# Kernel optimization log

Measured on AMD Instinct MI355X. Metric: run time of the kernel, lower is better.

The kernel has to match this reference:

```python
import jax, jax.numpy as jnp
import numpy as np

TEMPERATURE = 0.07
N, D, NUM_CLASSES = 8192, 1024, 128


def setup_inputs() -> dict:
    key = jax.random.key(0)
    k1, k2 = jax.random.split(key)
    embeddings = jax.random.normal(k1, (N, D), dtype=jnp.float32)
    labels = jax.random.randint(k2, (N,), 0, NUM_CLASSES, dtype=jnp.int64)
    return {"embeddings": embeddings, "labels": labels}


def reference(embeddings, labels):
    # L2-normalize rows (eps matches F.normalize default clamp of 1e-12 on the norm)
    norm = jnp.maximum(jnp.linalg.norm(embeddings, axis=-1, keepdims=True), 1e-12)
    emb = embeddings / norm
    # [N, N] similarity scaled by temperature
    sim = jnp.matmul(emb, emb.T) / TEMPERATURE
    # positive mask: same label, diagonal zeroed
    pos_mask = (labels[:, None] == labels[None, :]).astype(sim.dtype)
    pos_mask = pos_mask * (1.0 - jnp.eye(sim.shape[0], dtype=sim.dtype))
    exp_sim = jnp.exp(sim)
    sum_exp = exp_sim.sum(axis=1)              # [N]
    pos_sum = (exp_sim * pos_mask).sum(axis=1)  # [N]
    loss = -jnp.log(pos_sum / sum_exp)
    return loss.mean()
```

## Files before the change

### kernel.cpp

```cpp
#include <hip/hip_runtime.h>
#include <hip/hip_bf16.h>
#include <math.h>

#define N 8192
#define D 1024
#define BM 256
#define BK 64
#define NQUART 64
#define NFULL 512
#define NBLK (NQUART + NFULL)
#define ITERS 8

typedef __bf16 bf16_t;
typedef bf16_t bf16x4 __attribute__((ext_vector_type(4)));
typedef bf16_t bf16x8 __attribute__((ext_vector_type(8)));
typedef float f32x4 __attribute__((ext_vector_type(4)));

__global__ __launch_bounds__(256) void norm_cast(const float* __restrict__ in,
                                                 bf16_t* __restrict__ out,
                                                 float* __restrict__ sumExp,
                                                 float* __restrict__ posSum) {
    const int wave = threadIdx.x >> 6, lane = threadIdx.x & 63;
    const int row  = blockIdx.x * 4 + wave;
    const float4* src = (const float4*)(in + (size_t)row * D);
    float4 v[4];
    float ss = 0.f;
    #pragma unroll
    for (int i = 0; i < 4; ++i) {
        v[i] = src[lane + 64 * i];
        ss += v[i].x * v[i].x + v[i].y * v[i].y + v[i].z * v[i].z + v[i].w * v[i].w;
    }
    #pragma unroll
    for (int off = 32; off >= 1; off >>= 1) ss += __shfl_xor(ss, off, 64);
    const float scale = 1.0f / fmaxf(sqrtf(ss), 1e-12f);
    bf16x4* dst = (bf16x4*)(out + (size_t)row * D);
    #pragma unroll
    for (int i = 0; i < 4; ++i) {
        bf16x4 o;
        o[0] = (bf16_t)(v[i].x * scale);
        o[1] = (bf16_t)(v[i].y * scale);
        o[2] = (bf16_t)(v[i].z * scale);
        o[3] = (bf16_t)(v[i].w * scale);
        dst[lane + 64 * i] = o;
    }
    if (lane == 0) { sumExp[row] = 0.f; posSum[row] = 0.f; }
}

__global__ __launch_bounds__(512, 2) void gemm_fused(const bf16_t* __restrict__ E,
                                                     const int* __restrict__ labels,
                                                     float* __restrict__ sumExp,
                                                     float* __restrict__ posSum) {
    __shared__ bf16_t As[2][2][128 * 64];
    __shared__ bf16_t Bs[2][2][128 * 64];

    const int tid  = threadIdx.x;
    const int wave = tid >> 6;
    const int lane = tid & 63;
    const int lr   = lane & 15;
    const int q    = lane >> 4;
    const float invT = 1.0f / 0.07f;

    const int su0 = ((0 + q) ^ (lane & 7)) * 16;
    const int su1 = ((4 + q) ^ (lane & 7)) * 16;

    #define PHASE_MID() do {                                                             \
        __builtin_amdgcn_s_barrier();                                                    \
        asm volatile("s_waitcnt lgkmcnt(0)");                                            \
        __builtin_amdgcn_sched_barrier(0);                                               \
        __builtin_amdgcn_s_setprio(1);                                                   \
    } while (0)
    #define PHASE_END() do {                                                             \
        __builtin_amdgcn_s_setprio(0);                                                   \
        __builtin_amdgcn_s_barrier();                                                    \
    } while (0)

    if (blockIdx.x >= NFULL) {
        const int qb = (int)blockIdx.x - NFULL;
        const int p  = qb >> 2, qd = qb & 3;
        const int rowStart = 31 * BM + (qd >> 1) * 128;
        const int colStart = p * BM + (qd & 1) * 128;
        const int wm2 = wave >> 2;
        const int wn2 = wave & 3;
        char* Aflat = (char*)&As[0][0][0];
        char* Bflat = (char*)&Bs[0][0][0];

        f32x4 acc[4][2];
        #pragma unroll
        for (int m = 0; m < 4; ++m) { acc[m][0] = {0,0,0,0}; acc[m][1] = {0,0,0,0}; }

        const int r0 = tid >> 4;
        const int lu = (tid & 15) ^ (r0 & 7);
        const char* gA = (const char*)(E + (size_t)rowStart * D) + (size_t)r0 * 2048 + lu * 16;
        const char* gB = (const char*)(E + (size_t)colStart * D) + (size_t)r0 * 2048 + lu * 16;

        #define Q128STAGE(bi, t) do {                                                    \
            const char* ga_ = gA + (t) * 256;                                            \
            const char* gb_ = gB + (t) * 256;                                            \
            char* la_ = Aflat + (bi) * 32768 + wave * 1024;                              \
            char* lb_ = Bflat + (bi) * 32768 + wave * 1024;                              \
            _Pragma("unroll")                                                            \
            for (int g_ = 0; g_ < 4; ++g_) {                                             \
                __builtin_amdgcn_global_load_lds(                                        \
                    (const __attribute__((address_space(1))) void*)(ga_ + g_ * 32 * 2048), \
                    (__attribute__((address_space(3))) void*)(la_ + g_ * 8192), 16, 0, 0); \
                __builtin_amdgcn_global_load_lds(                                        \
                    (const __attribute__((address_space(1))) void*)(gb_ + g_ * 32 * 2048), \
                    (__attribute__((address_space(3))) void*)(lb_ + g_ * 8192), 16, 0, 0); \
            }                                                                            \
        } while (0)

        Q128STAGE(0, 0);
        asm volatile("s_waitcnt vmcnt(0)" ::: "memory");
        __builtin_amdgcn_sched_barrier(0);
        __builtin_amdgcn_s_barrier();

        #pragma unroll 1
        for (int s = 0; s < 8; ++s) {
            const int buf = s & 1;
            if (s < 7) Q128STAGE(buf ^ 1, s + 1);
            const char* aB = Aflat + buf * 32768 + (wm2 * 64 + lr) * 256;
            const char* bB = Bflat + buf * 32768 + (wn2 * 32 + lr) * 256;
            #pragma unroll
            for (int kc = 0; kc < 4; ++kc) {
                const int su_ = ((kc * 4 + q) ^ (lane & 7)) * 16;
                bf16x8 qa[4], qbv[2];
                #pragma unroll
                for (int m_ = 0; m_ < 4; ++m_)
                    qa[m_] = *(const bf16x8*)(aB + m_ * 4096 + su_);
                qbv[0] = *(const bf16x8*)(bB + su_);
                qbv[1] = *(const bf16x8*)(bB + 4096 + su_);
                #pragma unroll
                for (int m_ = 0; m_ < 4; ++m_) {
                    #pragma unroll
                    for (int n_ = 0; n_ < 2; ++n_)
                        acc[m_][n_] = __builtin_amdgcn_mfma_f32_16x16x32_bf16(
                            qa[m_], qbv[n_], acc[m_][n_], 0, 0, 0);
                }
            }
            asm volatile("s_waitcnt vmcnt(0)" ::: "memory");
            __builtin_amdgcn_sched_barrier(0);
            __builtin_amdgcn_s_barrier();
        }

        int lc[2];
        lc[0] = labels[colStart + wn2 * 32 + lr];
        lc[1] = labels[colStart + wn2 * 32 + 16 + lr];
        float colAll[2] = {0.f, 0.f}, colPos[2] = {0.f, 0.f};
        #pragma unroll
        for (int m = 0; m < 4; ++m) {
            #pragma unroll
            for (int e = 0; e < 4; ++e) {
                const int gi = rowStart + wm2 * 64 + m * 16 + q * 4 + e;
                const int li = labels[gi];
                float s_all = 0.f, s_pos = 0.f;
                #pragma unroll
                for (int n = 0; n < 2; ++n) {
                    const float v = __expf(acc[m][n][e] * invT);
                    const bool same = (lc[n] == li);
                    s_all += v;
                    if (same) s_pos += v;
                    colAll[n] += v;
                    if (same) colPos[n] += v;
                }
                #pragma unroll
                for (int off = 1; off < 16; off <<= 1) {
                    s_all += __shfl_xor(s_all, off, 64);
                    s_pos += __shfl_xor(s_pos, off, 64);
                }
                if (lr == 0) {
                    atomicAdd(&sumExp[gi], s_all);
                    atomicAdd(&posSum[gi], s_pos);
                }
            }
        }
        #pragma unroll
        for (int n = 0; n < 2; ++n) {
            float a = colAll[n], pp = colPos[n];
            a += __shfl_xor(a, 16, 64);  a += __shfl_xor(a, 32, 64);
            pp += __shfl_xor(pp, 16, 64); pp += __shfl_xor(pp, 32, 64);
            if (q == 0) {
                const int gj = colStart + wn2 * 32 + n * 16 + lr;
                atomicAdd(&sumExp[gj], a);
                atomicAdd(&posSum[gj], pp);
            }
        }
        return;
    }

    const int f0 = (int)blockIdx.x;
    const int f  = (f0 & 7) * (NFULL / 8) + (f0 >> 3);
    const int b  = (f < 496) ? f : f + 16;

    int ti = (int)((sqrtf(8.0f * (float)b + 1.0f) - 1.0f) * 0.5f);
    while ((ti + 1) * (ti + 2) / 2 <= b) ++ti;
    while (ti * (ti + 1) / 2 > b) --ti;
    const int tj = b - ti * (ti + 1) / 2;
    const bool isDiag = (ti == tj);

    const int wm   = wave >> 2;
    const int wn   = wave & 3;
    const int rowStart = ti * BM;
    const int colStart = tj * BM;

    f32x4 acc[8][4];
    #pragma unroll
    for (int m = 0; m < 8; ++m)
        #pragma unroll
        for (int n = 0; n < 4; ++n) acc[m][n] = {0.f, 0.f, 0.f, 0.f};

    const int r0  = tid >> 3;
    const int lu0 = (tid & 7) ^ (r0 & 7);
    const char* gA = (const char*)(E + (size_t)rowStart * D) + (size_t)r0 * (D * 2) + lu0 * 16;
    const char* gB = (const char*)(E + (size_t)colStart * D) + (size_t)r0 * (D * 2) + lu0 * 16;

    #define STAGE_A(buf, h, kb) do {                                                     \
        const char* g0_ = gA + (size_t)(h) * (128 * 2048) + (kb);                        \
        char* l0_ = (char*)&As[buf][h][0] + wave * 1024;                                 \
        __builtin_amdgcn_global_load_lds((const __attribute__((address_space(1))) void*)g0_, \
            (__attribute__((address_space(3))) void*)l0_, 16, 0, 0);                     \
        __builtin_amdgcn_global_load_lds(                                                \
            (const __attribute__((address_space(1))) void*)(g0_ + 64 * 2048),            \
            (__attribute__((address_space(3))) void*)(l0_ + 8192), 16, 0, 0);            \
    } while (0)
    #define STAGE_B(buf, h, kb) do {                                                     \
        const char* g0_ = gB + (size_t)(h) * (128 * 2048) + (kb);                        \
        char* l0_ = (char*)&Bs[buf][h][0] + wave * 1024;                                 \
        __builtin_amdgcn_global_load_lds((const __attribute__((address_space(1))) void*)g0_, \
            (__attribute__((address_space(3))) void*)l0_, 16, 0, 0);                     \
        __builtin_amdgcn_global_load_lds(                                                \
            (const __attribute__((address_space(1))) void*)(g0_ + 64 * 2048),            \
            (__attribute__((address_space(3))) void*)(l0_ + 8192), 16, 0, 0);            \
    } while (0)

    const char* rA0 = (const char*)&As[0][wm][0] + lr * 128;
    const char* rA1 = (const char*)&As[1][wm][0] + lr * 128;
    const char* rB0 = (const char*)&Bs[0][wn >> 1][0] + (wn & 1) * 8192 + lr * 128;
    const char* rB1 = (const char*)&Bs[1][wn >> 1][0] + (wn & 1) * 8192 + lr * 128;

    #define LD_A4(DST, RBASE, MOFFB, SU) do {                                            \
        _Pragma("unroll")                                                                \
        for (int m_ = 0; m_ < 4; ++m_)                                                   \
            DST[m_] = *(const bf16x8*)((RBASE) + (MOFFB) + m_ * 2048 + (SU));            \
    } while (0)
    #define LD_B4(DST, RBASE, SU) do {                                                   \
        _Pragma("unroll")                                                                \
        for (int n_ = 0; n_ < 4; ++n_)                                                   \
            DST[n_] = *(const bf16x8*)((RBASE) + n_ * 2048 + (SU));                      \
    } while (0)
    #define MFMA_QUAD(AF, BF, MO) do {                                                   \
        _Pragma("unroll")                                                                \
        for (int m_ = 0; m_ < 4; ++m_) {                                                 \
            _Pragma("unroll")                                                            \
            for (int n_ = 0; n_ < 4; ++n_)                                               \
                acc[(MO) + m_][n_] = __builtin_amdgcn_mfma_f32_16x16x32_bf16(            \
                    AF[m_], BF[n_], acc[(MO) + m_][n_], 0, 0, 0);                        \
        }                                                                                \
    } while (0)

    bf16x8 a0[4], a1[4], bq0[4], bq1[4];

    STAGE_B(0, 0, 0);  STAGE_B(0, 1, 0);
    STAGE_A(0, 0, 0);  STAGE_A(0, 1, 0);
    STAGE_B(1, 0, 128); STAGE_B(1, 1, 128);
    asm volatile("s_waitcnt vmcnt(4)" ::: "memory");
    __builtin_amdgcn_sched_barrier(0);
    __builtin_amdgcn_s_barrier();

    #pragma unroll 1
    for (int it = 0; it < ITERS; ++it) {
        const bool lastIt = (it == ITERS - 1);
        const int kb1 = (2 * it + 1) * 128;
        const int kb2 = (2 * it + 2) * 128;
        const int kb3 = (2 * it + 3) * 128;

        LD_A4(a0, rA0, 0, su0);
        LD_B4(bq0, rB0, su0);
        STAGE_A(1, 0, kb1);
        PHASE_MID();
        MFMA_QUAD(a0, bq0, 0);
        PHASE_END();

        LD_A4(a1, rA0, 0, su1);
        LD_B4(bq1, rB0, su1);
        STAGE_A(1, 1, kb1);
        PHASE_MID();
        MFMA_QUAD(a1, bq1, 0);
        PHASE_END();

        LD_A4(a0, rA0, 8192, su0);
        if (!lastIt) STAGE_B(0, 0, kb2);
        PHASE_MID();
        MFMA_QUAD(a0, bq0, 4);
        PHASE_END();

        LD_A4(a1, rA0, 8192, su1);
        if (!lastIt) {
            STAGE_B(0, 1, kb2);
            asm volatile("s_waitcnt vmcnt(4)" ::: "memory");
        } else {
            asm volatile("s_waitcnt vmcnt(0)" ::: "memory");
        }
        __builtin_amdgcn_sched_barrier(0);
        PHASE_MID();
        MFMA_QUAD(a1, bq1, 4);
        PHASE_END();

        LD_A4(a0, rA1, 0, su0);
        LD_B4(bq0, rB1, su0);
        if (!lastIt) STAGE_A(0, 0, kb2);
        PHASE_MID();
        MFMA_QUAD(a0, bq0, 0);
        PHASE_END();

        LD_A4(a1, rA1, 0, su1);
        LD_B4(bq1, rB1, su1);
        if (!lastIt) STAGE_A(0, 1, kb2);
        PHASE_MID();
        MFMA_QUAD(a1, bq1, 0);
        PHASE_END();

        LD_A4(a0, rA1, 8192, su0);
        if (!lastIt) STAGE_B(1, 0, kb3);
        PHASE_MID();
        MFMA_QUAD(a0, bq0, 4);
        PHASE_END();

        LD_A4(a1, rA1, 8192, su1);
        if (!lastIt) {
            STAGE_B(1, 1, kb3);
            asm volatile("s_waitcnt vmcnt(4)" ::: "memory");
            __builtin_amdgcn_sched_barrier(0);
        }
        PHASE_MID();
        MFMA_QUAD(a1, bq1, 4);
        PHASE_END();
    }

    int lc[4];
    #pragma unroll
    for (int n = 0; n < 4; ++n)
        lc[n] = labels[colStart + wn * 64 + n * 16 + lr];

    float colAll[4] = {0.f, 0.f, 0.f, 0.f};
    float colPos[4] = {0.f, 0.f, 0.f, 0.f};
    #pragma unroll
    for (int m = 0; m < 8; ++m) {
        #pragma unroll
        for (int e = 0; e < 4; ++e) {
            const int rloc = wm * 128 + m * 16 + q * 4 + e;
            const int gi   = rowStart + rloc;
            const int li   = labels[gi];
            float s_all = 0.f, s_pos = 0.f;
            #pragma unroll
            for (int n = 0; n < 4; ++n) {
                const int cloc = wn * 64 + n * 16 + lr;
                const int gj   = colStart + cloc;
                const float v  = __expf(acc[m][n][e] * invT);
                const bool same = (lc[n] == li);
                s_all += v;
                if (same && gi != gj) s_pos += v;
                if (!isDiag) {
                    colAll[n] += v;
                    if (same) colPos[n] += v;
                }
            }
            #pragma unroll
            for (int off = 1; off < 16; off <<= 1) {
                s_all += __shfl_xor(s_all, off, 64);
                s_pos += __shfl_xor(s_pos, off, 64);
            }
            if (lr == 0) {
                atomicAdd(&sumExp[gi], s_all);
                atomicAdd(&posSum[gi], s_pos);
            }
        }
    }
    if (!isDiag) {
        #pragma unroll
        for (int n = 0; n < 4; ++n) {
            float a = colAll[n], p = colPos[n];
            a += __shfl_xor(a, 16, 64);  a += __shfl_xor(a, 32, 64);
            p += __shfl_xor(p, 16, 64);  p += __shfl_xor(p, 32, 64);
            if (q == 0) {
                const int gj = colStart + wn * 64 + n * 16 + lr;
                atomicAdd(&sumExp[gj], a);
                atomicAdd(&posSum[gj], p);
            }
        }
    }
}

__global__ __launch_bounds__(1024) void finalize(const float* __restrict__ sumExp,
                                                 const float* __restrict__ posSum,
                                                 float* __restrict__ out) {
    const int tid = threadIdx.x;
    float s = 0.f;
    #pragma unroll
    for (int i = tid; i < N; i += 1024)
        s += __logf(sumExp[i] / posSum[i]);
    #pragma unroll
    for (int off = 32; off >= 1; off >>= 1) s += __shfl_xor(s, off, 64);
    __shared__ float red[16];
    if ((tid & 63) == 0) red[tid >> 6] = s;
    __syncthreads();
    if (tid == 0) {
        float t = 0.f;
        #pragma unroll
        for (int i = 0; i < 16; ++i) t += red[i];
        out[0] = t / (float)N;
    }
}

extern "C" void kernel_launch(void* const* d_in, const int* in_sizes, int n_in,
                              void* d_out, int out_size, void* d_ws, size_t ws_size,
                              hipStream_t stream) {
    const float* emb    = (const float*)d_in[0];
    const int*   labels = (const int*)d_in[1];
    float* out = (float*)d_out;

    float*  sumExp = (float*)d_ws;
    float*  posSum = sumExp + N;
    bf16_t* EN     = (bf16_t*)((char*)d_ws + (size_t)2 * N * sizeof(float));

    norm_cast<<<N / 4, 256, 0, stream>>>(emb, EN, sumExp, posSum);

    gemm_fused<<<NBLK, 512, 0, stream>>>(EN, labels, sumExp, posSum);

    finalize<<<1, 1024, 0, stream>>>(sumExp, posSum, out);
}
```

Before: 208.2 us.

## Split quarter-tile blocks into separate kernel with 4-stage BK=64 pipeline

The 128x128 quarter-tile work is moved out of the fused GEMM into its own kernel, launched after the full-tile kernel. The new kernel uses a 4-slot shared-memory ring with BK=64 stages and keeps three loads in flight, with finer vmcnt waits and setprio around the MFMA block. Splitting removes the branch and the register and LDS pressure that the quarter path put on the full-tile kernel. The cost is an extra launch and a serialized tail: the 64 quarter blocks no longer fill idle CUs alongside the full tiles.

Result: slower. 224.6 us (+7.9%).

```diff
diff --git a/kernel.cpp b/kernel.cpp
--- a/kernel.cpp
+++ b/kernel.cpp
@@ -8,7 +8,6 @@
 #define BK 64
 #define NQUART 64
 #define NFULL 512
-#define NBLK (NQUART + NFULL)
 #define ITERS 8
 
 typedef __bf16 bf16_t;
@@ -46,10 +45,21 @@
     if (lane == 0) { sumExp[row] = 0.f; posSum[row] = 0.f; }
 }
 
-__global__ __launch_bounds__(512, 2) void gemm_fused(const bf16_t* __restrict__ E,
-                                                     const int* __restrict__ labels,
-                                                     float* __restrict__ sumExp,
-                                                     float* __restrict__ posSum) {
+#define PHASE_MID() do {                                                             \
+    __builtin_amdgcn_s_barrier();                                                    \
+    asm volatile("s_waitcnt lgkmcnt(0)");                                            \
+    __builtin_amdgcn_sched_barrier(0);                                               \
+    __builtin_amdgcn_s_setprio(1);                                                   \
+} while (0)
+#define PHASE_END() do {                                                             \
+    __builtin_amdgcn_s_setprio(0);                                                   \
+    __builtin_amdgcn_s_barrier();                                                    \
+} while (0)
+
+__global__ __launch_bounds__(512, 2) void gemm_full(const bf16_t* __restrict__ E,
+                                                    const int* __restrict__ labels,
+                                                    float* __restrict__ sumExp,
+                                                    float* __restrict__ posSum) {
     __shared__ bf16_t As[2][2][128 * 64];
     __shared__ bf16_t Bs[2][2][128 * 64];
 
@@ -62,130 +72,6 @@
 
     const int su0 = ((0 + q) ^ (lane & 7)) * 16;
     const int su1 = ((4 + q) ^ (lane & 7)) * 16;
-
-    #define PHASE_MID() do {                                                             \
-        __builtin_amdgcn_s_barrier();                                                    \
-        asm volatile("s_waitcnt lgkmcnt(0)");                                            \
-        __builtin_amdgcn_sched_barrier(0);                                               \
-        __builtin_amdgcn_s_setprio(1);                                                   \
-    } while (0)
-    #define PHASE_END() do {                                                             \
-        __builtin_amdgcn_s_setprio(0);                                                   \
-        __builtin_amdgcn_s_barrier();                                                    \
-    } while (0)
-
-    if (blockIdx.x >= NFULL) {
-        const int qb = (int)blockIdx.x - NFULL;
-        const int p  = qb >> 2, qd = qb & 3;
-        const int rowStart = 31 * BM + (qd >> 1) * 128;
-        const int colStart = p * BM + (qd & 1) * 128;
-        const int wm2 = wave >> 2;
-        const int wn2 = wave & 3;
-        char* Aflat = (char*)&As[0][0][0];
-        char* Bflat = (char*)&Bs[0][0][0];
-
-        f32x4 acc[4][2];
-        #pragma unroll
-        for (int m = 0; m < 4; ++m) { acc[m][0] = {0,0,0,0}; acc[m][1] = {0,0,0,0}; }
-
-        const int r0 = tid >> 4;
-        const int lu = (tid & 15) ^ (r0 & 7);
-        const char* gA = (const char*)(E + (size_t)rowStart * D) + (size_t)r0 * 2048 + lu * 16;
-        const char* gB = (const char*)(E + (size_t)colStart * D) + (size_t)r0 * 2048 + lu * 16;
-
-        #define Q128STAGE(bi, t) do {                                                    \
-            const char* ga_ = gA + (t) * 256;                                            \
-            const char* gb_ = gB + (t) * 256;                                            \
-            char* la_ = Aflat + (bi) * 32768 + wave * 1024;                              \
-            char* lb_ = Bflat + (bi) * 32768 + wave * 1024;                              \
-            _Pragma("unroll")                                                            \
-            for (int g_ = 0; g_ < 4; ++g_) {                                             \
-                __builtin_amdgcn_global_load_lds(                                        \
-                    (const __attribute__((address_space(1))) void*)(ga_ + g_ * 32 * 2048), \
-                    (__attribute__((address_space(3))) void*)(la_ + g_ * 8192), 16, 0, 0); \
-                __builtin_amdgcn_global_load_lds(                                        \
-                    (const __attribute__((address_space(1))) void*)(gb_ + g_ * 32 * 2048), \
-                    (__attribute__((address_space(3))) void*)(lb_ + g_ * 8192), 16, 0, 0); \
-            }                                                                            \
-        } while (0)
-
-        Q128STAGE(0, 0);
-        asm volatile("s_waitcnt vmcnt(0)" ::: "memory");
-        __builtin_amdgcn_sched_barrier(0);
-        __builtin_amdgcn_s_barrier();
-
-        #pragma unroll 1
-        for (int s = 0; s < 8; ++s) {
-            const int buf = s & 1;
-            if (s < 7) Q128STAGE(buf ^ 1, s + 1);
-            const char* aB = Aflat + buf * 32768 + (wm2 * 64 + lr) * 256;
-            const char* bB = Bflat + buf * 32768 + (wn2 * 32 + lr) * 256;
-            #pragma unroll
-            for (int kc = 0; kc < 4; ++kc) {
-                const int su_ = ((kc * 4 + q) ^ (lane & 7)) * 16;
-                bf16x8 qa[4], qbv[2];
-                #pragma unroll
-                for (int m_ = 0; m_ < 4; ++m_)
-                    qa[m_] = *(const bf16x8*)(aB + m_ * 4096 + su_);
-                qbv[0] = *(const bf16x8*)(bB + su_);
-                qbv[1] = *(const bf16x8*)(bB + 4096 + su_);
-                #pragma unroll
-                for (int m_ = 0; m_ < 4; ++m_) {
-                    #pragma unroll
-                    for (int n_ = 0; n_ < 2; ++n_)
-                        acc[m_][n_] = __builtin_amdgcn_mfma_f32_16x16x32_bf16(
-                            qa[m_], qbv[n_], acc[m_][n_], 0, 0, 0);
-                }
-            }
-            asm volatile("s_waitcnt vmcnt(0)" ::: "memory");
-            __builtin_amdgcn_sched_barrier(0);
-            __builtin_amdgcn_s_barrier();
-        }
-
-        int lc[2];
-        lc[0] = labels[colStart + wn2 * 32 + lr];
-        lc[1] = labels[colStart + wn2 * 32 + 16 + lr];
-        float colAll[2] = {0.f, 0.f}, colPos[2] = {0.f, 0.f};
-        #pragma unroll
-        for (int m = 0; m < 4; ++m) {
-            #pragma unroll
-            for (int e = 0; e < 4; ++e) {
-                const int gi = rowStart + wm2 * 64 + m * 16 + q * 4 + e;
-                const int li = labels[gi];
-                float s_all = 0.f, s_pos = 0.f;
-                #pragma unroll
-                for (int n = 0; n < 2; ++n) {
-                    const float v = __expf(acc[m][n][e] * invT);
-                    const bool same = (lc[n] == li);
-                    s_all += v;
-                    if (same) s_pos += v;
-                    colAll[n] += v;
-                    if (same) colPos[n] += v;
-                }
-                #pragma unroll
-                for (int off = 1; off < 16; off <<= 1) {
-                    s_all += __shfl_xor(s_all, off, 64);
-                    s_pos += __shfl_xor(s_pos, off, 64);
-                }
-                if (lr == 0) {
-                    atomicAdd(&sumExp[gi], s_all);
-                    atomicAdd(&posSum[gi], s_pos);
-                }
-            }
-        }
-        #pragma unroll
-        for (int n = 0; n < 2; ++n) {
-            float a = colAll[n], pp = colPos[n];
-            a += __shfl_xor(a, 16, 64);  a += __shfl_xor(a, 32, 64);
-            pp += __shfl_xor(pp, 16, 64); pp += __shfl_xor(pp, 32, 64);
-            if (q == 0) {
-                const int gj = colStart + wn2 * 32 + n * 16 + lr;
-                atomicAdd(&sumExp[gj], a);
-                atomicAdd(&posSum[gj], pp);
-            }
-        }
-        return;
-    }
 
     const int f0 = (int)blockIdx.x;
     const int f  = (f0 & 7) * (NFULL / 8) + (f0 >> 3);
@@ -390,6 +276,148 @@
     }
 }
 
+__global__ __launch_bounds__(512, 2) void gemm_quart(const bf16_t* __restrict__ E,
+                                                     const int* __restrict__ labels,
+                                                     float* __restrict__ sumExp,
+                                                     float* __restrict__ posSum) {
+    __shared__ bf16_t As[4][128 * 64];
+    __shared__ bf16_t Bs[4][128 * 64];
+
+    const int tid  = threadIdx.x;
+    const int wave = tid >> 6;
+    const int lane = tid & 63;
+    const int lr   = lane & 15;
+    const int q    = lane >> 4;
+    const float invT = 1.0f / 0.07f;
+
+    const int qb = (int)blockIdx.x;
+    const int p  = qb >> 2, qd = qb & 3;
+    const int rowStart = 31 * BM + (qd >> 1) * 128;
+    const int colStart = p * BM + (qd & 1) * 128;
+    const int wm2 = wave >> 2;
+    const int wn2 = wave & 3;
+
+    f32x4 acc[4][2];
+    #pragma unroll
+    for (int m = 0; m < 4; ++m) { acc[m][0] = {0,0,0,0}; acc[m][1] = {0,0,0,0}; }
+
+    const int r0  = tid >> 3;
+    const int lu0 = (tid & 7) ^ (r0 & 7);
+    const char* gA = (const char*)(E + (size_t)rowStart * D) + (size_t)r0 * (D * 2) + lu0 * 16;
+    const char* gB = (const char*)(E + (size_t)colStart * D) + (size_t)r0 * (D * 2) + lu0 * 16;
+
+    #define QST(slot, kb) do {                                                           \
+        const char* ga_ = gA + (kb);                                                     \
+        const char* gb_ = gB + (kb);                                                     \
+        char* la_ = (char*)&As[slot][0] + wave * 1024;                                   \
+        char* lb_ = (char*)&Bs[slot][0] + wave * 1024;                                   \
+        __builtin_amdgcn_global_load_lds((const __attribute__((address_space(1))) void*)ga_, \
+            (__attribute__((address_space(3))) void*)la_, 16, 0, 0);                     \
+        __builtin_amdgcn_global_load_lds(                                                \
+            (const __attribute__((address_space(1))) void*)(ga_ + 64 * 2048),            \
+            (__attribute__((address_space(3))) void*)(la_ + 8192), 16, 0, 0);            \
+        __builtin_amdgcn_global_load_lds((const __attribute__((address_space(1))) void*)gb_, \
+            (__attribute__((address_space(3))) void*)lb_, 16, 0, 0);                     \
+        __builtin_amdgcn_global_load_lds(                                                \
+            (const __attribute__((address_space(1))) void*)(gb_ + 64 * 2048),            \
+            (__attribute__((address_space(3))) void*)(lb_ + 8192), 16, 0, 0);            \
+    } while (0)
+
+    const int su0 = ((0 + q) ^ (lane & 7)) * 16;
+    const int su1 = ((4 + q) ^ (lane & 7)) * 16;
+
+    QST(0, 0);
+    QST(1, 128);
+    QST(2, 256);
+    asm volatile("s_waitcnt vmcnt(8)" ::: "memory");
+    __builtin_amdgcn_sched_barrier(0);
+    __builtin_amdgcn_s_barrier();
+
+    #pragma unroll 1
+    for (int s = 0; s < 16; ++s) {
+        const int slot = s & 3;
+        if (s <= 12) QST((s + 3) & 3, (s + 3) * 128);
+        const char* aB = (const char*)&As[slot][0] + (wm2 * 64 + lr) * 128;
+        const char* bB = (const char*)&Bs[slot][0] + (wn2 * 32 + lr) * 128;
+        bf16x8 qa0[4], qa1[4], qb0v[2], qb1v[2];
+        #pragma unroll
+        for (int m_ = 0; m_ < 4; ++m_) {
+            qa0[m_] = *(const bf16x8*)(aB + m_ * 2048 + su0);
+            qa1[m_] = *(const bf16x8*)(aB + m_ * 2048 + su1);
+        }
+        qb0v[0] = *(const bf16x8*)(bB + su0);
+        qb0v[1] = *(const bf16x8*)(bB + 2048 + su0);
+        qb1v[0] = *(const bf16x8*)(bB + su1);
+        qb1v[1] = *(const bf16x8*)(bB + 2048 + su1);
+        asm volatile("s_waitcnt lgkmcnt(0)");
+        __builtin_amdgcn_sched_barrier(0);
+        __builtin_amdgcn_s_setprio(1);
+        #pragma unroll
+        for (int m_ = 0; m_ < 4; ++m_) {
+            #pragma unroll
+            for (int n_ = 0; n_ < 2; ++n_)
+                acc[m_][n_] = __builtin_amdgcn_mfma_f32_16x16x32_bf16(
+                    qa0[m_], qb0v[n_], acc[m_][n_], 0, 0, 0);
+        }
+        #pragma unroll
+        for (int m_ = 0; m_ < 4; ++m_) {
+            #pragma unroll
+            for (int n_ = 0; n_ < 2; ++n_)
+                acc[m_][n_] = __builtin_amdgcn_mfma_f32_16x16x32_bf16(
+                    qa1[m_], qb1v[n_], acc[m_][n_], 0, 0, 0);
+        }
+        __builtin_amdgcn_s_setprio(0);
+        if (s <= 12)      asm volatile("s_waitcnt vmcnt(8)" ::: "memory");
+        else if (s == 13) asm volatile("s_waitcnt vmcnt(4)" ::: "memory");
+        else              asm volatile("s_waitcnt vmcnt(0)" ::: "memory");
+        __builtin_amdgcn_sched_barrier(0);
+        __builtin_amdgcn_s_barrier();
+    }
+
+    int lc[2];
+    lc[0] = labels[colStart + wn2 * 32 + lr];
+    lc[1] = labels[colStart + wn2 * 32 + 16 + lr];
+    float colAll[2] = {0.f, 0.f}, colPos[2] = {0.f, 0.f};
+    #pragma unroll
+    for (int m = 0; m < 4; ++m) {
+        #pragma unroll
+        for (int e = 0; e < 4; ++e) {
+            const int gi = rowStart + wm2 * 64 + m * 16 + q * 4 + e;
+            const int li = labels[gi];
+            float s_all = 0.f, s_pos = 0.f;
+            #pragma unroll
+            for (int n = 0; n < 2; ++n) {
+                const float v = __expf(acc[m][n][e] * invT);
+                const bool same = (lc[n] == li);
+                s_all += v;
+                if (same) s_pos += v;
+                colAll[n] += v;
+                if (same) colPos[n] += v;
+            }
+            #pragma unroll
+            for (int off = 1; off < 16; off <<= 1) {
+                s_all += __shfl_xor(s_all, off, 64);
+                s_pos += __shfl_xor(s_pos, off, 64);
+            }
+            if (lr == 0) {
+                atomicAdd(&sumExp[gi], s_all);
+                atomicAdd(&posSum[gi], s_pos);
+            }
+        }
+    }
+    #pragma unroll
+    for (int n = 0; n < 2; ++n) {
+        float a = colAll[n], pp = colPos[n];
+        a += __shfl_xor(a, 16, 64);  a += __shfl_xor(a, 32, 64);
+        pp += __shfl_xor(pp, 16, 64); pp += __shfl_xor(pp, 32, 64);
+        if (q == 0) {
+            const int gj = colStart + wn2 * 32 + n * 16 + lr;
+            atomicAdd(&sumExp[gj], a);
+            atomicAdd(&posSum[gj], pp);
+        }
+    }
+}
+
 __global__ __launch_bounds__(1024) void finalize(const float* __restrict__ sumExp,
                                                  const float* __restrict__ posSum,
                                                  float* __restrict__ out) {
@@ -424,7 +452,8 @@
 
     norm_cast<<<N / 4, 256, 0, stream>>>(emb, EN, sumExp, posSum);
 
-    gemm_fused<<<NBLK, 512, 0, stream>>>(EN, labels, sumExp, posSum);
+    gemm_full<<<NFULL, 512, 0, stream>>>(EN, labels, sumExp, posSum);
+    gemm_quart<<<NQUART, 512, 0, stream>>>(EN, labels, sumExp, posSum);
 
     finalize<<<1, 1024, 0, stream>>>(sumExp, posSum, out);
 }
```
